# Kernel optimization log

Hardware: AMD Instinct MI355X
Metric: run time of the kernel (lower is better)

The kernel has to match this reference:

```python
import jax, jax.numpy as jnp
import numpy as np

M, OUT, IN = 16384, 2048, 2048

def setup_inputs() -> dict:
    key = jax.random.key(0)
    k1, k2 = jax.random.split(key)
    x = jax.random.normal(k1, (M, IN), dtype=jnp.float32)
    weight = jax.random.normal(k2, (OUT, IN), dtype=jnp.float32)  # nn.Linear weight [out, in]
    alpha = jnp.ones((1,), dtype=jnp.float32) * 0.5
    return {"x": x, "weight": weight, "alpha": alpha}

def reference(x, weight, alpha):
    # DualRateAlphaFunction forward: binarize weight to sign(w) and scale by learned alpha.
    binary_weight = jnp.sign(weight) * alpha  # [out, in]
    # F.linear(x, binary_weight): x @ binary_weight.T
    return jnp.einsum('mi,oi->mo', x, binary_weight)
```

## Files before the change

### kernel.cpp

```cpp
#include <hip/hip_runtime.h>
#include <stdint.h>
#include <type_traits>

#define M_DIM 16384
#define N_DIM 2048
#define K_DIM 2048

typedef __bf16 bf16_t;
typedef __bf16 bf16x8 __attribute__((ext_vector_type(8)));
typedef __bf16 bf16x4 __attribute__((ext_vector_type(4)));
typedef float f32x4 __attribute__((ext_vector_type(4)));

template <int N> using ic = std::integral_constant<int, N>;

__device__ __forceinline__ void gload_lds16(const void* g, void* l) {
  __builtin_amdgcn_global_load_lds(
      (const __attribute__((address_space(1))) void*)g,
      (__attribute__((address_space(3))) void*)l, 16, 0, 0);
}

template <bool SIGN>
__global__ void cvt_kernel(const float* __restrict__ in, bf16_t* __restrict__ out) {
  long long i = ((long long)blockIdx.x * 256 + threadIdx.x) * 8;
  const float4* p = (const float4*)(in + i);
  float4 v0 = p[0];
  float4 v1 = p[1];
  float f[8] = {v0.x, v0.y, v0.z, v0.w, v1.x, v1.y, v1.z, v1.w};
  bf16x8 r;
#pragma unroll
  for (int j = 0; j < 8; ++j) {
    float v = f[j];
    if (SIGN) v = (v > 0.f) ? 1.f : ((v < 0.f) ? -1.f : 0.f);
    r[j] = (bf16_t)v;
  }
  *(bf16x8*)(out + i) = r;
}

__global__ __launch_bounds__(512, 2) void gemm8p(const bf16_t* __restrict__ A,
                                                 const bf16_t* __restrict__ B,
                                                 const float* __restrict__ alpha_p,
                                                 float* __restrict__ C) {
  extern __shared__ char smem[];

  const int tid = threadIdx.x;
  const int lane = tid & 63;
  const int wid = tid >> 6;
  const int wm = wid >> 2;
  const int wn = wid & 3;

  const int bid = blockIdx.x;
  const int swz = (bid & 7) * 64 + (bid >> 3);
  const int bm = swz >> 3;
  const int bn = swz & 7;

  const int q = lane >> 4;
  const int r15 = lane & 15;

  const int swc = (r15 & 7) << 4;
  int aoff[2], boff[2];
#pragma unroll
  for (int k = 0; k < 2; ++k) {
    int ck = (k * 64 + q * 16) ^ swc;
    aoff[k] = (wm * 128 + r15) * 128 + ck;
    boff[k] = 32768 + (wn * 64 + r15) * 128 + ck;
  }

  const char* asrc[4];
  const char* bsrc[4];
  int adsto[4], bdsto[4];
#pragma unroll
  for (int j = 0; j < 4; ++j) {
    int P = j * 8192 + tid * 16;
    int row = P >> 7;
    int lcol = (P & 127) ^ ((row & 7) << 4);
    asrc[j] = (const char*)A + (size_t)(bm * 256 + row) * (K_DIM * 2) + lcol;
    bsrc[j] = (const char*)B + (size_t)(bn * 256 + row) * (K_DIM * 2) + lcol;
    adsto[j] = j * 8192 + wid * 1024;
    bdsto[j] = 32768 + j * 8192 + wid * 1024;
  }

  f32x4 acc[8][4];
#pragma unroll
  for (int mt = 0; mt < 8; ++mt)
#pragma unroll
    for (int nt = 0; nt < 4; ++nt) acc[mt][nt] = (f32x4){0.f, 0.f, 0.f, 0.f};

#pragma unroll
  for (int t = 0; t < 2; ++t) {
#pragma unroll
    for (int j = 0; j < 4; ++j)
      gload_lds16(asrc[j] + t * 128, smem + t * 65536 + adsto[j]);
#pragma unroll
    for (int j = 0; j < 4; ++j)
      gload_lds16(bsrc[j] + t * 128, smem + t * 65536 + bdsto[j]);
  }
  asm volatile("s_waitcnt vmcnt(8)" ::: "memory");
  __builtin_amdgcn_s_barrier();

  auto kstep = [&](auto UC, auto MC) {
    constexpr int U = UC.value;
    constexpr int MODE = MC.value;
    constexpr int TB = U * 65536;
    constexpr int GOFF = (U + 2) * 128;

    bf16x8 a[4][2], bL[2][2], bH[2][2];

#pragma unroll
    for (int mt = 0; mt < 4; ++mt)
#pragma unroll
      for (int k = 0; k < 2; ++k)
        a[mt][k] = *(const bf16x8*)(smem + TB + aoff[k] + mt * 2048);
#pragma unroll
    for (int nt = 0; nt < 2; ++nt)
#pragma unroll
      for (int k = 0; k < 2; ++k)
        bL[nt][k] = *(const bf16x8*)(smem + TB + boff[k] + nt * 2048);
    __builtin_amdgcn_s_barrier();
    asm volatile("s_waitcnt lgkmcnt(0)" ::: "memory");
    __builtin_amdgcn_s_setprio(1);
#pragma unroll
    for (int k = 0; k < 2; ++k)
#pragma unroll
      for (int mt = 0; mt < 4; ++mt)
#pragma unroll
        for (int nt = 0; nt < 2; ++nt)
          acc[mt][nt] = __builtin_amdgcn_mfma_f32_16x16x32_bf16(
              a[mt][k], bL[nt][k], acc[mt][nt], 0, 0, 0);
    __builtin_amdgcn_s_setprio(0);
    __builtin_amdgcn_s_barrier();

#pragma unroll
    for (int nt = 0; nt < 2; ++nt)
#pragma unroll
      for (int k = 0; k < 2; ++k)
        bH[nt][k] = *(const bf16x8*)(smem + TB + boff[k] + (2 + nt) * 2048);
    __builtin_amdgcn_s_barrier();
    asm volatile("s_waitcnt lgkmcnt(0)" ::: "memory");
    __builtin_amdgcn_s_setprio(1);
#pragma unroll
    for (int k = 0; k < 2; ++k)
#pragma unroll
      for (int mt = 0; mt < 4; ++mt)
#pragma unroll
        for (int nt = 0; nt < 2; ++nt)
          acc[mt][2 + nt] = __builtin_amdgcn_mfma_f32_16x16x32_bf16(
              a[mt][k], bH[nt][k], acc[mt][2 + nt], 0, 0, 0);
    __builtin_amdgcn_s_setprio(0);
    __builtin_amdgcn_s_barrier();

#pragma unroll
    for (int mt = 0; mt < 4; ++mt)
#pragma unroll
      for (int k = 0; k < 2; ++k)
        a[mt][k] = *(const bf16x8*)(smem + TB + aoff[k] + (4 + mt) * 2048);
    if constexpr (MODE == 0) {
#pragma unroll
      for (int j = 0; j < 4; ++j)
        gload_lds16(bsrc[j] + GOFF, smem + TB + bdsto[j]);
    }
    __builtin_amdgcn_s_barrier();
    asm volatile("s_waitcnt lgkmcnt(0)" ::: "memory");
    __builtin_amdgcn_s_setprio(1);
#pragma unroll
    for (int k = 0; k < 2; ++k)
#pragma unroll
      for (int mt = 0; mt < 4; ++mt)
#pragma unroll
        for (int nt = 0; nt < 2; ++nt)
          acc[4 + mt][2 + nt] = __builtin_amdgcn_mfma_f32_16x16x32_bf16(
              a[mt][k], bH[nt][k], acc[4 + mt][2 + nt], 0, 0, 0);
    __builtin_amdgcn_s_setprio(0);
    __builtin_amdgcn_s_barrier();

    if constexpr (MODE == 0) {
#pragma unroll
      for (int j = 0; j < 4; ++j)
        gload_lds16(asrc[j] + GOFF, smem + TB + adsto[j]);
      asm volatile("s_waitcnt vmcnt(8)" ::: "memory");
    } else if constexpr (MODE == 1) {
      asm volatile("s_waitcnt vmcnt(0)" ::: "memory");
    }
    __builtin_amdgcn_s_barrier();
    __builtin_amdgcn_s_setprio(1);
#pragma unroll
    for (int k = 0; k < 2; ++k)
#pragma unroll
      for (int mt = 0; mt < 4; ++mt)
#pragma unroll
        for (int nt = 0; nt < 2; ++nt)
          acc[4 + mt][nt] = __builtin_amdgcn_mfma_f32_16x16x32_bf16(
              a[mt][k], bL[nt][k], acc[4 + mt][nt], 0, 0, 0);
    __builtin_amdgcn_s_setprio(0);
    __builtin_amdgcn_s_barrier();
  };

#pragma unroll 1
  for (int T = 0; T < 15; ++T) {
    kstep(ic<0>{}, ic<0>{});
    kstep(ic<1>{}, ic<0>{});
#pragma unroll
    for (int j = 0; j < 4; ++j) { asrc[j] += 256; bsrc[j] += 256; }
  }
  kstep(ic<0>{}, ic<1>{});
  kstep(ic<1>{}, ic<2>{});

  const float alpha = alpha_p[0];
  const int rbase = bm * 256 + wm * 128 + q * 4;
  const int cbase = bn * 256 + wn * 64 + r15;
#pragma unroll
  for (int mt = 0; mt < 8; ++mt)
#pragma unroll
    for (int nt = 0; nt < 4; ++nt)
#pragma unroll
      for (int r = 0; r < 4; ++r)
        C[(size_t)(rbase + mt * 16 + r) * N_DIM + cbase + nt * 16] =
            alpha * acc[mt][nt][r];
}

__global__ __launch_bounds__(256) void gemm_fallback(const float* __restrict__ Ap,
                                                     const float* __restrict__ Bp,
                                                     const float* __restrict__ alpha_p,
                                                     float* __restrict__ C) {
  __shared__ bf16_t Asf[128 * 32];
  __shared__ bf16_t Bsf[128 * 32];
  const int tid = threadIdx.x;
  const int lane = tid & 63;
  const int wid = tid >> 6;
  const int wr = wid >> 1;
  const int wc = wid & 1;
  const int cpx = gridDim.x >> 3;
  const int bid = blockIdx.x;
  const int swz = (bid & 7) * cpx + (bid >> 3);
  const int NB = N_DIM / 128;
  const int bm = swz / NB;
  const int bn = swz % NB;
  f32x4 acc[4][4];
#pragma unroll
  for (int m = 0; m < 4; ++m)
#pragma unroll
    for (int n = 0; n < 4; ++n) acc[m][n] = (f32x4){0.f, 0.f, 0.f, 0.f};
  const int r0 = lane & 15;
  const int ko = (lane >> 4) * 8;
  for (int kk = 0; kk < K_DIM; kk += 32) {
    const float* Af = Ap + (size_t)bm * 128 * K_DIM + kk;
    const float* Bf = Bp + (size_t)bn * 128 * K_DIM + kk;
#pragma unroll
    for (int qq = 0; qq < 4; ++qq) {
      int e = qq * 256 + tid;
      int row = e >> 3;
      int kc = (e & 7) << 2;
      float4 v = *(const float4*)(Af + (size_t)row * K_DIM + kc);
      bf16x4 tv;
      tv[0] = (bf16_t)v.x; tv[1] = (bf16_t)v.y; tv[2] = (bf16_t)v.z; tv[3] = (bf16_t)v.w;
      *(bf16x4*)&Asf[e * 4] = tv;
    }
#pragma unroll
    for (int qq = 0; qq < 4; ++qq) {
      int e = qq * 256 + tid;
      int row = e >> 3;
      int kc = (e & 7) << 2;
      float4 v = *(const float4*)(Bf + (size_t)row * K_DIM + kc);
      float s[4] = {v.x, v.y, v.z, v.w};
      bf16x4 tv;
#pragma unroll
      for (int j = 0; j < 4; ++j)
        tv[j] = (bf16_t)((s[j] > 0.f) ? 1.f : ((s[j] < 0.f) ? -1.f : 0.f));
      *(bf16x4*)&Bsf[e * 4] = tv;
    }
    __syncthreads();
    bf16x8 a[4], b[4];
#pragma unroll
    for (int m = 0; m < 4; ++m) a[m] = *(const bf16x8*)&Asf[(wr * 64 + m * 16 + r0) * 32 + ko];
#pragma unroll
    for (int n = 0; n < 4; ++n) b[n] = *(const bf16x8*)&Bsf[(wc * 64 + n * 16 + r0) * 32 + ko];
#pragma unroll
    for (int m = 0; m < 4; ++m)
#pragma unroll
      for (int n = 0; n < 4; ++n)
        acc[m][n] = __builtin_amdgcn_mfma_f32_16x16x32_bf16(a[m], b[n], acc[m][n], 0, 0, 0);
    __syncthreads();
  }
  const float alpha = alpha_p[0];
  const int rowb = bm * 128 + wr * 64 + (lane >> 4) * 4;
  const int colb = bn * 128 + wc * 64 + r0;
#pragma unroll
  for (int m = 0; m < 4; ++m)
#pragma unroll
    for (int n = 0; n < 4; ++n)
#pragma unroll
      for (int r = 0; r < 4; ++r)
        C[(size_t)(rowb + m * 16 + r) * N_DIM + colb + n * 16] = alpha * acc[m][n][r];
}

extern "C" void kernel_launch(void* const* d_in, const int* in_sizes, int n_in,
                              void* d_out, int out_size, void* d_ws, size_t ws_size,
                              hipStream_t stream) {
  const float* x = (const float*)d_in[0];
  const float* w = (const float*)d_in[1];
  const float* alpha = (const float*)d_in[2];
  float* out = (float*)d_out;

  const size_t nx = (size_t)M_DIM * K_DIM;
  const size_t nw = (size_t)N_DIM * K_DIM;
  const size_t need = (nx + nw) * sizeof(bf16_t);

  if (ws_size >= need) {
    bf16_t* xb = (bf16_t*)d_ws;
    bf16_t* wb = xb + nx;
    cvt_kernel<false><<<(int)(nx / 2048), 256, 0, stream>>>(x, xb);
    cvt_kernel<true><<<(int)(nw / 2048), 256, 0, stream>>>(w, wb);
    (void)hipFuncSetAttribute((const void*)gemm8p,
                              hipFuncAttributeMaxDynamicSharedMemorySize, 131072);
    gemm8p<<<512, 512, 131072, stream>>>(xb, wb, alpha, out);
  } else {
    gemm_fallback<<<(M_DIM / 128) * (N_DIM / 128), 256, 0, stream>>>(x, w, alpha, out);
  }
}
```

Before: 168.5 us.

## Fuse conversion kernels, interleave global loads across phases, add sched barriers

Merges the two fp32-to-bf16 conversion launches into one kernel, which removes a launch and its tail. Inside the GEMM, the next tile's A and B global-to-LDS loads are spread across the MFMA phases instead of being issued in two bursts. B rows are reordered in LDS so the low and high halves of each wave's columns sit in separate contiguous regions. Scheduling barriers and an early partial lgkmcnt wait are added to pin the instruction order, at the risk of limiting compiler scheduling.

```diff
diff --git a/kernel.cpp b/kernel.cpp
--- a/kernel.cpp
+++ b/kernel.cpp
@@ -13,15 +13,24 @@
 
 template <int N> using ic = std::integral_constant<int, N>;
 
+#define SB0() __builtin_amdgcn_sched_barrier(0)
+
 __device__ __forceinline__ void gload_lds16(const void* g, void* l) {
   __builtin_amdgcn_global_load_lds(
       (const __attribute__((address_space(1))) void*)g,
       (__attribute__((address_space(3))) void*)l, 16, 0, 0);
 }
 
-template <bool SIGN>
-__global__ void cvt_kernel(const float* __restrict__ in, bf16_t* __restrict__ out) {
-  long long i = ((long long)blockIdx.x * 256 + threadIdx.x) * 8;
+#define NXB (M_DIM * K_DIM / 2048)
+#define NWB (N_DIM * K_DIM / 2048)
+__global__ void cvt_fused(const float* __restrict__ x, const float* __restrict__ w,
+                          bf16_t* __restrict__ xb, bf16_t* __restrict__ wb) {
+  int b = blockIdx.x;
+  const float* in = (b < NXB) ? x : w;
+  bf16_t* out = (b < NXB) ? xb : wb;
+  bool sign = (b >= NXB);
+  if (b >= NXB) b -= NXB;
+  long long i = ((long long)b * 256 + threadIdx.x) * 8;
   const float4* p = (const float4*)(in + i);
   float4 v0 = p[0];
   float4 v1 = p[1];
@@ -30,13 +39,13 @@
 #pragma unroll
   for (int j = 0; j < 8; ++j) {
     float v = f[j];
-    if (SIGN) v = (v > 0.f) ? 1.f : ((v < 0.f) ? -1.f : 0.f);
+    if (sign) v = (v > 0.f) ? 1.f : ((v < 0.f) ? -1.f : 0.f);
     r[j] = (bf16_t)v;
   }
   *(bf16x8*)(out + i) = r;
 }
 
-__global__ __launch_bounds__(512, 2) void gemm8p(const bf16_t* __restrict__ A,
+__global__ __launch_bounds__(512, 2) void gemm12(const bf16_t* __restrict__ A,
                                                  const bf16_t* __restrict__ B,
                                                  const float* __restrict__ alpha_p,
                                                  float* __restrict__ C) {
@@ -57,27 +66,34 @@
   const int r15 = lane & 15;
 
   const int swc = (r15 & 7) << 4;
-  int aoff[2], boff[2];
+  int aoff[2], boffL[2], boffH[2];
 #pragma unroll
   for (int k = 0; k < 2; ++k) {
     int ck = (k * 64 + q * 16) ^ swc;
     aoff[k] = (wm * 128 + r15) * 128 + ck;
-    boff[k] = 32768 + (wn * 64 + r15) * 128 + ck;
-  }
-
-  const char* asrc[4];
-  const char* bsrc[4];
-  int adsto[4], bdsto[4];
-#pragma unroll
-  for (int j = 0; j < 4; ++j) {
-    int P = j * 8192 + tid * 16;
+    boffL[k] = 32768 + (wn * 32 + r15) * 128 + ck;
+    boffH[k] = 32768 + 16384 + (wn * 32 + r15) * 128 + ck;
+  }
+
+  const char* asrc0;
+  {
+    int P = tid * 16;
     int row = P >> 7;
     int lcol = (P & 127) ^ ((row & 7) << 4);
-    asrc[j] = (const char*)A + (size_t)(bm * 256 + row) * (K_DIM * 2) + lcol;
-    bsrc[j] = (const char*)B + (size_t)(bn * 256 + row) * (K_DIM * 2) + lcol;
-    adsto[j] = j * 8192 + wid * 1024;
-    bdsto[j] = 32768 + j * 8192 + wid * 1024;
-  }
+    asrc0 = (const char*)A + (size_t)(bm * 256 + row) * (K_DIM * 2) + lcol;
+  }
+  const char* bsrc[4];
+#pragma unroll
+  for (int c = 0; c < 4; ++c) {
+    int P = c * 8192 + tid * 16;
+    int lr = P >> 7;
+    int grow;
+    if (lr < 128) grow = (lr >> 5) * 64 + (lr & 31);
+    else { int l2 = lr - 128; grow = (l2 >> 5) * 64 + 32 + (l2 & 31); }
+    int lcol = (P & 127) ^ ((lr & 7) << 4);
+    bsrc[c] = (const char*)B + (size_t)(bn * 256 + grow) * (K_DIM * 2) + lcol;
+  }
+  const int dsto = wid * 1024;
 
   f32x4 acc[8][4];
 #pragma unroll
@@ -89,13 +105,16 @@
   for (int t = 0; t < 2; ++t) {
 #pragma unroll
     for (int j = 0; j < 4; ++j)
-      gload_lds16(asrc[j] + t * 128, smem + t * 65536 + adsto[j]);
-#pragma unroll
-    for (int j = 0; j < 4; ++j)
-      gload_lds16(bsrc[j] + t * 128, smem + t * 65536 + bdsto[j]);
+      gload_lds16(asrc0 + (size_t)j * 262144 + t * 128,
+                  smem + t * 65536 + j * 8192 + dsto);
+#pragma unroll
+    for (int c = 0; c < 4; ++c)
+      gload_lds16(bsrc[c] + t * 128, smem + t * 65536 + 32768 + c * 8192 + dsto);
   }
   asm volatile("s_waitcnt vmcnt(8)" ::: "memory");
+  SB0();
   __builtin_amdgcn_s_barrier();
+  SB0();
 
   auto kstep = [&](auto UC, auto MC) {
     constexpr int U = UC.value;
@@ -114,9 +133,12 @@
     for (int nt = 0; nt < 2; ++nt)
 #pragma unroll
       for (int k = 0; k < 2; ++k)
-        bL[nt][k] = *(const bf16x8*)(smem + TB + boff[k] + nt * 2048);
+        bL[nt][k] = *(const bf16x8*)(smem + TB + boffL[k] + nt * 2048);
+    asm volatile("s_waitcnt lgkmcnt(8)" ::: "memory");
+    SB0();
     __builtin_amdgcn_s_barrier();
     asm volatile("s_waitcnt lgkmcnt(0)" ::: "memory");
+    SB0();
     __builtin_amdgcn_s_setprio(1);
 #pragma unroll
     for (int k = 0; k < 2; ++k)
@@ -127,15 +149,24 @@
           acc[mt][nt] = __builtin_amdgcn_mfma_f32_16x16x32_bf16(
               a[mt][k], bL[nt][k], acc[mt][nt], 0, 0, 0);
     __builtin_amdgcn_s_setprio(0);
+    SB0();
     __builtin_amdgcn_s_barrier();
 
 #pragma unroll
     for (int nt = 0; nt < 2; ++nt)
 #pragma unroll
       for (int k = 0; k < 2; ++k)
-        bH[nt][k] = *(const bf16x8*)(smem + TB + boff[k] + (2 + nt) * 2048);
+        bH[nt][k] = *(const bf16x8*)(smem + TB + boffH[k] + nt * 2048);
+    if constexpr (MODE == 0) {
+      gload_lds16(asrc0 + 0 * 262144 + GOFF, smem + TB + 0 * 8192 + dsto);
+      gload_lds16(asrc0 + 2 * 262144 + GOFF, smem + TB + 2 * 8192 + dsto);
+      gload_lds16(bsrc[0] + GOFF, smem + TB + 32768 + 0 * 8192 + dsto);
+      gload_lds16(bsrc[1] + GOFF, smem + TB + 32768 + 1 * 8192 + dsto);
+    }
+    SB0();
     __builtin_amdgcn_s_barrier();
     asm volatile("s_waitcnt lgkmcnt(0)" ::: "memory");
+    SB0();
     __builtin_amdgcn_s_setprio(1);
 #pragma unroll
     for (int k = 0; k < 2; ++k)
@@ -146,6 +177,7 @@
           acc[mt][2 + nt] = __builtin_amdgcn_mfma_f32_16x16x32_bf16(
               a[mt][k], bH[nt][k], acc[mt][2 + nt], 0, 0, 0);
     __builtin_amdgcn_s_setprio(0);
+    SB0();
     __builtin_amdgcn_s_barrier();
 
 #pragma unroll
@@ -154,12 +186,13 @@
       for (int k = 0; k < 2; ++k)
         a[mt][k] = *(const bf16x8*)(smem + TB + aoff[k] + (4 + mt) * 2048);
     if constexpr (MODE == 0) {
-#pragma unroll
-      for (int j = 0; j < 4; ++j)
-        gload_lds16(bsrc[j] + GOFF, smem + TB + bdsto[j]);
-    }
+      gload_lds16(bsrc[2] + GOFF, smem + TB + 32768 + 2 * 8192 + dsto);
+      gload_lds16(bsrc[3] + GOFF, smem + TB + 32768 + 3 * 8192 + dsto);
+    }
+    SB0();
     __builtin_amdgcn_s_barrier();
     asm volatile("s_waitcnt lgkmcnt(0)" ::: "memory");
+    SB0();
     __builtin_amdgcn_s_setprio(1);
 #pragma unroll
     for (int k = 0; k < 2; ++k)
@@ -170,17 +203,19 @@
           acc[4 + mt][2 + nt] = __builtin_amdgcn_mfma_f32_16x16x32_bf16(
               a[mt][k], bH[nt][k], acc[4 + mt][2 + nt], 0, 0, 0);
     __builtin_amdgcn_s_setprio(0);
+    SB0();
     __builtin_amdgcn_s_barrier();
 
     if constexpr (MODE == 0) {
-#pragma unroll
-      for (int j = 0; j < 4; ++j)
-        gload_lds16(asrc[j] + GOFF, smem + TB + adsto[j]);
+      gload_lds16(asrc0 + 1 * 262144 + GOFF, smem + TB + 1 * 8192 + dsto);
+      gload_lds16(asrc0 + 3 * 262144 + GOFF, smem + TB + 3 * 8192 + dsto);
       asm volatile("s_waitcnt vmcnt(8)" ::: "memory");
     } else if constexpr (MODE == 1) {
       asm volatile("s_waitcnt vmcnt(0)" ::: "memory");
     }
-    __builtin_amdgcn_s_barrier();
+    SB0();
+    __builtin_amdgcn_s_barrier();
+    SB0();
     __builtin_amdgcn_s_setprio(1);
 #pragma unroll
     for (int k = 0; k < 2; ++k)
@@ -191,6 +226,7 @@
           acc[4 + mt][nt] = __builtin_amdgcn_mfma_f32_16x16x32_bf16(
               a[mt][k], bL[nt][k], acc[4 + mt][nt], 0, 0, 0);
     __builtin_amdgcn_s_setprio(0);
+    SB0();
     __builtin_amdgcn_s_barrier();
   };
 
@@ -198,8 +234,9 @@
   for (int T = 0; T < 15; ++T) {
     kstep(ic<0>{}, ic<0>{});
     kstep(ic<1>{}, ic<0>{});
-#pragma unroll
-    for (int j = 0; j < 4; ++j) { asrc[j] += 256; bsrc[j] += 256; }
+    asrc0 += 256;
+#pragma unroll
+    for (int c = 0; c < 4; ++c) bsrc[c] += 256;
   }
   kstep(ic<0>{}, ic<1>{});
   kstep(ic<1>{}, ic<2>{});
@@ -307,11 +344,10 @@
   if (ws_size >= need) {
     bf16_t* xb = (bf16_t*)d_ws;
     bf16_t* wb = xb + nx;
-    cvt_kernel<false><<<(int)(nx / 2048), 256, 0, stream>>>(x, xb);
-    cvt_kernel<true><<<(int)(nw / 2048), 256, 0, stream>>>(w, wb);
-    (void)hipFuncSetAttribute((const void*)gemm8p,
+    cvt_fused<<<NXB + NWB, 256, 0, stream>>>(x, w, xb, wb);
+    (void)hipFuncSetAttribute((const void*)gemm12,
                               hipFuncAttributeMaxDynamicSharedMemorySize, 131072);
-    gemm8p<<<512, 512, 131072, stream>>>(xb, wb, alpha, out);
+    gemm12<<<512, 512, 131072, stream>>>(xb, wb, alpha, out);
   } else {
     gemm_fallback<<<(M_DIM / 128) * (N_DIM / 128), 256, 0, stream>>>(x, w, alpha, out);
   }
```

Measured after the change: 163.0 us (median of 3 runs). 3.3% less time.
